# Kernel optimization log

Measured on AMD Instinct MI355X. Metric: run time of the kernel, lower is better.

Reference implementation:

```python
import jax, jax.numpy as jnp
import numpy as np
from jax import lax

L = 12        # transformer layers
H = 768       # d_model
NH = 12       # heads
HD = H // NH  # head dim
F = 2048      # ffn dim (torch TransformerEncoderLayer default)
V = 128       # vocab_size (level logits)
NLV = 128     # n_levels (rows of routed weight W)
B, S = 8, 512
EPS = 1e-5


def _layer_norm(x, g, b):
    mu = jnp.mean(x, axis=-1, keepdims=True)
    var = jnp.mean(jnp.square(x - mu), axis=-1, keepdims=True)
    return g * (x - mu) / jnp.sqrt(var + EPS) + b


def _encoder(x, layer_params):
    # torch nn.TransformerEncoderLayer, post-LN, ReLU, eval mode (no dropout)
    def block(h, p):
        Wqkv, bqkv, Wo, bo, g1, bb1, W1, b1f, W2, b2f, g2, bb2 = p
        qkv = h @ Wqkv.T + bqkv                      # [B,S,3H]
        q, k, v = jnp.split(qkv, 3, axis=-1)
        sh = (h.shape[0], h.shape[1], NH, HD)
        q, k, v = q.reshape(sh), k.reshape(sh), v.reshape(sh)
        scores = jnp.einsum('bqhd,bkhd->bhqk', q, k) / jnp.sqrt(jnp.asarray(HD, h.dtype))
        attn = jax.nn.softmax(scores, axis=-1)
        o = jnp.einsum('bhqk,bkhd->bqhd', attn, v).reshape(h.shape)
        o = o @ Wo.T + bo
        h = _layer_norm(h + o, g1, bb1)
        f = jnp.maximum(h @ W1.T + b1f, 0.0) @ W2.T + b2f
        h = _layer_norm(h + f, g2, bb2)
        return h, None
    x, _ = lax.scan(block, x, layer_params)
    return x


def setup_inputs() -> dict:
    key = jax.random.key(0)
    ks = jax.random.split(key, 20)
    s = 0.02
    rn = lambda k, shp: jax.random.normal(k, shp, jnp.float32) * s
    inp = {
        'level_ids': jax.random.randint(ks[0], (B, S), 0, V, jnp.int32),
        'sublevel_ids': jax.random.randint(ks[1], (B, S), 0, V, jnp.int32),
        'bin_emb': rn(ks[2], (V, H)),
        'sub_emb': rn(ks[3], (V, H)),
        'Wqkv': rn(ks[4], (L, 3 * H, H)),
        'bqkv': jnp.zeros((L, 3 * H), jnp.float32),
        'Wo': rn(ks[5], (L, H, H)),
        'bo': jnp.zeros((L, H), jnp.float32),
        'ln1_g': jnp.ones((L, H), jnp.float32),
        'ln1_b': jnp.zeros((L, H), jnp.float32),
        'W1': rn(ks[6], (L, F, H)),
        'b1': jnp.zeros((L, F), jnp.float32),
        'W2': rn(ks[7], (L, H, F)),
        'b2': jnp.zeros((L, H), jnp.float32),
        'ln2_g': jnp.ones((L, H), jnp.float32),
        'ln2_b': jnp.zeros((L, H), jnp.float32),
        'W_lm': rn(ks[8], (V, H)),
        'b_lm': jnp.zeros((V,), jnp.float32),
        'W': rn(ks[9], (NLV, H, V)),       # routed per-level weights
        'bias': jnp.zeros((NLV, V), jnp.float32),
    }
    return inp


def reference(level_ids, sublevel_ids, bin_emb, sub_emb, Wqkv, bqkv, Wo, bo,
              ln1_g, ln1_b, W1, b1, W2, b2, ln2_g, ln2_b, W_lm, b_lm, W, bias):
    # embedding: sum of two id tables (tabular bin/subbin embedding)
    x = bin_emb[level_ids] + sub_emb[sublevel_ids]            # [B,S,H]
    layer_params = (Wqkv, bqkv, Wo, bo, ln1_g, ln1_b, W1, b1, W2, b2, ln2_g, ln2_b)
    x = _encoder(x, layer_params)                              # [B,S,H]
    out = x @ W_lm.T + b_lm                                    # [B,S,V]
    ix = jnp.argmax(out, axis=-1)                              # [B,S] routing index
    # per-token weight gather + batched vec-mat: the irregular hot path
    Wg = W[ix]                                                 # [B,S,H,V]
    sublevel_out = jnp.einsum('bsh,bshv->bsv', x, Wg) + bias[ix]
    return (out, sublevel_out)
```

## Files before the change

### kernel.cpp

```cpp
#include <hip/hip_runtime.h>
#include <cstdint>
#include <cstddef>

#define TOK 4096
#define HD_ 64
#define NH_ 12
#define H_ 768
#define F_ 2048
#define V_ 128
#define L_ 12
#define SEQ 512
#define BQKV (3*H_)
#define BATCH 8

typedef _Float16 f16;
typedef _Float16 f16x8 __attribute__((ext_vector_type(8)));
typedef _Float16 f16x4 __attribute__((ext_vector_type(4)));
typedef float    f32x4 __attribute__((ext_vector_type(4)));

#define GLDS16(g, l) __builtin_amdgcn_global_load_lds( \
    (const __attribute__((address_space(1))) uint32_t*)(g), \
    (__attribute__((address_space(3))) uint32_t*)(l), 16, 0, 0)

__device__ __forceinline__ float wave_sum(float v) {
#pragma unroll
  for (int m = 32; m >= 1; m >>= 1) v += __shfl_xor(v, m);
  return v;
}

__device__ __forceinline__ void split16(float v, f16& h, f16& lo) {
  h = (f16)v;
  lo = (f16)((v - (float)h) * 2048.0f);
}

__device__ __forceinline__ int swz(int r, int c) {
  int byte = (r << 7) + (c << 1);
  byte ^= (r & 7) << 4;
  return byte >> 1;
}

__global__ __launch_bounds__(256)
void k_convert(const float* __restrict__ src, f16* __restrict__ h, f16* __restrict__ l,
               int n4, float scale) {
  int i = blockIdx.x * 256 + threadIdx.x;
  int stride = gridDim.x * 256;
  for (; i < n4; i += stride) {
    float4 v = ((const float4*)src)[i];
    v.x *= scale; v.y *= scale; v.z *= scale; v.w *= scale;
    f16x4 vh, vl;
    f16 a, b;
    split16(v.x, a, b); vh[0] = a; vl[0] = b;
    split16(v.y, a, b); vh[1] = a; vl[1] = b;
    split16(v.z, a, b); vh[2] = a; vl[2] = b;
    split16(v.w, a, b); vh[3] = a; vl[3] = b;
    ((f16x4*)h)[i] = vh;
    ((f16x4*)l)[i] = vl;
  }
}

__global__ __launch_bounds__(256)
void k_embed2(const int* __restrict__ lid, const int* __restrict__ sid,
              const float* __restrict__ be, const float* __restrict__ se,
              float* __restrict__ x, f16* __restrict__ xh, f16* __restrict__ xl,
              int* __restrict__ counts) {
  int t = blockIdx.x;
  if (t == 0 && threadIdx.x < V_) counts[threadIdx.x] = 0;
  int li = lid[t], si = sid[t];
  const float* bp = be + (size_t)li * H_;
  const float* sp = se + (size_t)si * H_;
  size_t base = (size_t)t * H_;
#pragma unroll
  for (int j = 0; j < 3; ++j) {
    int hh = threadIdx.x + 256 * j;
    float v = bp[hh] + sp[hh];
    x[base + hh] = v;
    f16 a, b; split16(v, a, b);
    xh[base + hh] = a; xl[base + hh] = b;
  }
}

template<int BM, int BN, int MODE, int SPLIT>
__global__ __launch_bounds__(256, 2)
void k_gemm5(const f16* __restrict__ Ah, const f16* __restrict__ Al,
             const f16* __restrict__ Bh, const f16* __restrict__ Bl,
             const float* __restrict__ bias, float* __restrict__ C,
             f16* __restrict__ Ch, f16* __restrict__ Cl,
             int N, int K) {
  constexpr int MI = BM / 32, NJ = BN / 32;
  constexpr int IA = BM / 64, IB = BN / 64;
  constexpr int ABYT = BM * 64, BBYT = BN * 64;
  constexpr int BUFB = 2 * ABYT + 2 * BBYT;
  constexpr int NGL = 2 * (IA + IB);
  __shared__ __align__(16) char sm_[2 * BUFB];
  const int tid = threadIdx.x;
  const int lane = tid & 63, wid = tid >> 6;
  const int wr = wid >> 1, wc = wid & 1;

  const unsigned flat = blockIdx.x + gridDim.x * (blockIdx.y + gridDim.y * blockIdx.z);
  const unsigned G = gridDim.x >> 3;
  const unsigned xcd = flat & 7u;
  const unsigned idx = flat >> 3;
  const unsigned mt = xcd * G + idx % G;
  const unsigned rest = idx / G;
  const unsigned nt = rest % gridDim.y;
  const unsigned zt = rest / gridDim.y;

  const int bm = mt * BM, bn = nt * BN;
  const size_t rs = (size_t)K * 2;
  const size_t koff = (size_t)zt * (size_t)(K / SPLIT) * 2;

  const int srow = tid >> 2, schk = tid & 3;
  const char* ga[2][IA];
  const char* gb[2][IB];
#pragma unroll
  for (int u = 0; u < IA; ++u) {
    int row = u * 64 + srow;
    int c = schk ^ ((row >> 1) & 3);
    ga[0][u] = (const char*)Ah + (size_t)(bm + row) * rs + c * 16 + koff;
    ga[1][u] = (const char*)Al + (size_t)(bm + row) * rs + c * 16 + koff;
  }
#pragma unroll
  for (int u = 0; u < IB; ++u) {
    int row = u * 64 + srow;
    int c = schk ^ ((row >> 1) & 3);
    gb[0][u] = (const char*)Bh + (size_t)(bn + row) * rs + c * 16 + koff;
    gb[1][u] = (const char*)Bl + (size_t)(bn + row) * rs + c * 16 + koff;
  }

  const int rr = lane & 15, cgrp = lane >> 4;
  int aoff[MI][2], boff[NJ][2];
#pragma unroll
  for (int i = 0; i < MI; ++i) {
    int row = wr * (BM / 2) + i * 16 + rr;
    int sw = (cgrp ^ ((row >> 1) & 3)) * 16;
    aoff[i][0] = row * 64 + sw;
    aoff[i][1] = ABYT + row * 64 + sw;
  }
#pragma unroll
  for (int j = 0; j < NJ; ++j) {
    int row = wc * (BN / 2) + j * 16 + rr;
    int sw = (cgrp ^ ((row >> 1) & 3)) * 16;
    boff[j][0] = 2 * ABYT + row * 64 + sw;
    boff[j][1] = 2 * ABYT + BBYT + row * 64 + sw;
  }

  f32x4 aH[MI][NJ], aM[MI][NJ];
#pragma unroll
  for (int i = 0; i < MI; ++i)
#pragma unroll
    for (int j = 0; j < NJ; ++j)
#pragma unroll
      for (int q = 0; q < 4; ++q) { aH[i][j][q] = 0.0f; aM[i][j][q] = 0.0f; }

  auto STG = [&](char* bufbase) __attribute__((always_inline)) {
    char* base = bufbase + wid * 1024;
#pragma unroll
    for (int u = 0; u < IA; ++u) {
      GLDS16(ga[0][u], base + u * 4096);
      GLDS16(ga[1][u], base + ABYT + u * 4096);
      ga[0][u] += 64; ga[1][u] += 64;
    }
#pragma unroll
    for (int u = 0; u < IB; ++u) {
      GLDS16(gb[0][u], base + 2 * ABYT + u * 4096);
      GLDS16(gb[1][u], base + 2 * ABYT + BBYT + u * 4096);
      gb[0][u] += 64; gb[1][u] += 64;
    }
  };

  char* b0 = sm_;
  char* b1 = sm_ + BUFB;
  const int nst = (K / SPLIT) / 32;
  STG(b0);
  STG(b1);
  for (int s = 0; s < nst; ++s) {
    if (s < nst - 1) {
      asm volatile("s_waitcnt vmcnt(%0)" :: "i"(NGL) : "memory");
    } else {
      asm volatile("s_waitcnt vmcnt(0)" ::: "memory");
    }
    __builtin_amdgcn_s_barrier();
    __builtin_amdgcn_sched_barrier(0);
    const char* base = (s & 1) ? b1 : b0;
    f16x8 fb[NJ][2], fa[MI][2];
#pragma unroll
    for (int j = 0; j < NJ; ++j) {
      fb[j][0] = *(const f16x8*)(base + boff[j][0]);
      fb[j][1] = *(const f16x8*)(base + boff[j][1]);
    }
#pragma unroll
    for (int i = 0; i < MI; ++i) {
      fa[i][0] = *(const f16x8*)(base + aoff[i][0]);
      fa[i][1] = *(const f16x8*)(base + aoff[i][1]);
    }
    asm volatile("s_waitcnt lgkmcnt(0)" ::: "memory");
    __builtin_amdgcn_s_barrier();
    __builtin_amdgcn_sched_barrier(0);
    if (s + 2 < nst) STG((char*)base);
    __builtin_amdgcn_s_setprio(1);
#pragma unroll
    for (int i = 0; i < MI; ++i) {
#pragma unroll
      for (int j = 0; j < NJ; ++j) {
        aH[i][j] = __builtin_amdgcn_mfma_f32_16x16x32_f16(fa[i][0], fb[j][0], aH[i][j], 0, 0, 0);
        aM[i][j] = __builtin_amdgcn_mfma_f32_16x16x32_f16(fa[i][0], fb[j][1], aM[i][j], 0, 0, 0);
        aM[i][j] = __builtin_amdgcn_mfma_f32_16x16x32_f16(fa[i][1], fb[j][0], aM[i][j], 0, 0, 0);
      }
    }
    __builtin_amdgcn_s_setprio(0);
  }

  const int r4 = (lane >> 4) * 4, cc = lane & 15;
  float* Cp = (MODE == 3) ? (C + (size_t)zt * ((size_t)TOK * N)) : C;
#pragma unroll
  for (int i = 0; i < MI; ++i) {
#pragma unroll
    for (int j = 0; j < NJ; ++j) {
      int col = bn + wc * (BN / 2) + j * 16 + cc;
      float bz = (MODE == 3) ? 0.0f : bias[col];
#pragma unroll
      for (int q = 0; q < 4; ++q) {
        int row = bm + wr * (BM / 2) + i * 16 + r4 + q;
        float v = (aH[i][j][q] + aM[i][j][q] * (1.0f / 2048.0f)) * (1.0f / 64.0f) + bz;
        if (MODE == 0 || MODE == 3) {
          Cp[(size_t)row * N + col] = v;
        } else {
          if (MODE == 1) v = fmaxf(v, 0.0f);
          f16 a, b; split16(v, a, b);
          Ch[(size_t)row * N + col] = a;
          Cl[(size_t)row * N + col] = b;
        }
      }
    }
  }
}

__global__ __launch_bounds__(256)
void k_flash_mfma(const f16* __restrict__ ph, const f16* __restrict__ pl,
                  f16* __restrict__ oh, f16* __restrict__ ol) {
  __shared__ __align__(16) f16 VtH[4096];
  __shared__ __align__(16) f16 VtL[4096];
  __shared__ __align__(16) f16 PH[4096];
  __shared__ __align__(16) f16 PL[4096];
  __shared__ float PS[2][64];
  const int tid = threadIdx.x;
  const int lane = tid & 63, wid = tid >> 6;
  const int wr = wid >> 1, wc = wid & 1;
  const unsigned flat = blockIdx.x + 8u * blockIdx.y;
  const unsigned xcd = flat & 7u;
  const unsigned idx = flat >> 3;
  const int qt = idx & 7;
  const int bh = xcd * 12 + (idx >> 3);
  const int b = bh / NH_, hd = bh % NH_;
  const int rr = lane & 15, kg = (lane >> 4) * 8;
  const size_t tok0 = (size_t)b * SEQ;

  f16x8 qfh[2][2], qfl[2][2];
#pragma unroll
  for (int ifr = 0; ifr < 2; ++ifr)
#pragma unroll
    for (int ks = 0; ks < 2; ++ks) {
      size_t g = (tok0 + qt * 64 + wr * 32 + ifr * 16 + rr) * (size_t)BQKV + hd * HD_ + ks * 32 + kg;
      qfh[ifr][ks] = *(const f16x8*)&ph[g];
      qfl[ifr][ks] = *(const f16x8*)&pl[g];
    }

  f32x4 oha[2][2], oma[2][2];
  float psum[2] = {0.f, 0.f};
#pragma unroll
  for (int i = 0; i < 2; ++i)
#pragma unroll
    for (int j = 0; j < 2; ++j)
#pragma unroll
      for (int q = 0; q < 4; ++q) { oha[i][j][q] = 0.0f; oma[i][j][q] = 0.0f; }

  const int vj = tid >> 2;
  const int vs = tid & 3;

  for (int kt = 0; kt < SEQ / 64; ++kt) {
    __syncthreads();
#pragma unroll
    for (int s = 0; s < 2; ++s) {
      int d0 = (vs + s * 4) * 8;
      size_t g = (tok0 + kt * 64 + vj) * (size_t)BQKV + 2 * H_ + hd * HD_ + d0;
      f16x8 vh8 = *(const f16x8*)&ph[g];
      f16x8 vl8 = *(const f16x8*)&pl[g];
#pragma unroll
      for (int u = 0; u < 8; ++u) {
        VtH[swz(d0 + u, vj)] = vh8[u];
        VtL[swz(d0 + u, vj)] = vl8[u];
      }
    }
    __syncthreads();
    f16x8 kfh[2][2], kfl[2][2];
#pragma unroll
    for (int jf = 0; jf < 2; ++jf)
#pragma unroll
      for (int ks = 0; ks < 2; ++ks) {
        size_t g = (tok0 + kt * 64 + wc * 32 + jf * 16 + rr) * (size_t)BQKV + H_ + hd * HD_ + ks * 32 + kg;
        kfh[jf][ks] = *(const f16x8*)&ph[g];
        kfl[jf][ks] = *(const f16x8*)&pl[g];
      }
    f32x4 sh[2][2], sm2[2][2];
#pragma unroll
    for (int j = 0; j < 2; ++j)
#pragma unroll
      for (int i = 0; i < 2; ++i)
#pragma unroll
        for (int q = 0; q < 4; ++q) { sh[j][i][q] = 0.0f; sm2[j][i][q] = 0.0f; }
    __builtin_amdgcn_s_setprio(1);
#pragma unroll
    for (int jf = 0; jf < 2; ++jf)
#pragma unroll
      for (int ifr = 0; ifr < 2; ++ifr)
#pragma unroll
        for (int ks = 0; ks < 2; ++ks) {
          sh[jf][ifr]  = __builtin_amdgcn_mfma_f32_16x16x32_f16(kfh[jf][ks], qfh[ifr][ks], sh[jf][ifr], 0, 0, 0);
          sm2[jf][ifr] = __builtin_amdgcn_mfma_f32_16x16x32_f16(kfl[jf][ks], qfh[ifr][ks], sm2[jf][ifr], 0, 0, 0);
          sm2[jf][ifr] = __builtin_amdgcn_mfma_f32_16x16x32_f16(kfh[jf][ks], qfl[ifr][ks], sm2[jf][ifr], 0, 0, 0);
        }
    __builtin_amdgcn_s_setprio(0);
#pragma unroll
    for (int ifr = 0; ifr < 2; ++ifr) {
#pragma unroll
      for (int jf = 0; jf < 2; ++jf) {
        f16x4 v4h, v4l;
#pragma unroll
        for (int q = 0; q < 4; ++q) {
          float sval = (sh[jf][ifr][q] + sm2[jf][ifr][q] * (1.0f / 2048.0f)) * 0.125f;
          float p = expf(sval);
          psum[ifr] += p;
          f16 a, b2; split16(p, a, b2);
          v4h[q] = a; v4l[q] = b2;
        }
        int qi = wr * 32 + ifr * 16 + rr;
        int j0 = wc * 32 + jf * 16 + (lane >> 4) * 4;
        *(f16x4*)&PH[swz(qi, j0)] = v4h;
        *(f16x4*)&PL[swz(qi, j0)] = v4l;
      }
    }
    __syncthreads();
#pragma unroll
    for (int ks = 0; ks < 2; ++ks) {
      f16x8 pfh[2], pfl[2], vfh[2], vfl[2];
#pragma unroll
      for (int ifr = 0; ifr < 2; ++ifr) {
        pfh[ifr] = *(const f16x8*)&PH[swz(wr * 32 + ifr * 16 + rr, ks * 32 + kg)];
        pfl[ifr] = *(const f16x8*)&PL[swz(wr * 32 + ifr * 16 + rr, ks * 32 + kg)];
      }
#pragma unroll
      for (int jf = 0; jf < 2; ++jf) {
        vfh[jf] = *(const f16x8*)&VtH[swz(wc * 32 + jf * 16 + rr, ks * 32 + kg)];
        vfl[jf] = *(const f16x8*)&VtL[swz(wc * 32 + jf * 16 + rr, ks * 32 + kg)];
      }
      __builtin_amdgcn_s_setprio(1);
#pragma unroll
      for (int ifr = 0; ifr < 2; ++ifr)
#pragma unroll
        for (int jf = 0; jf < 2; ++jf) {
          oha[ifr][jf] = __builtin_amdgcn_mfma_f32_16x16x32_f16(pfh[ifr], vfh[jf], oha[ifr][jf], 0, 0, 0);
          oma[ifr][jf] = __builtin_amdgcn_mfma_f32_16x16x32_f16(pfh[ifr], vfl[jf], oma[ifr][jf], 0, 0, 0);
          oma[ifr][jf] = __builtin_amdgcn_mfma_f32_16x16x32_f16(pfl[ifr], vfh[jf], oma[ifr][jf], 0, 0, 0);
        }
      __builtin_amdgcn_s_setprio(0);
    }
  }

#pragma unroll
  for (int ifr = 0; ifr < 2; ++ifr) {
    psum[ifr] += __shfl_xor(psum[ifr], 16);
    psum[ifr] += __shfl_xor(psum[ifr], 32);
  }
  if (lane < 16) {
    PS[wc][wr * 32 + lane]      = psum[0];
    PS[wc][wr * 32 + 16 + lane] = psum[1];
  }
  __syncthreads();

#pragma unroll
  for (int ifr = 0; ifr < 2; ++ifr)
#pragma unroll
    for (int jf = 0; jf < 2; ++jf)
#pragma unroll
      for (int q = 0; q < 4; ++q) {
        int i = wr * 32 + ifr * 16 + (lane >> 4) * 4 + q;
        float inv = 1.0f / (PS[0][i] + PS[1][i]);
        float o = (oha[ifr][jf][q] + oma[ifr][jf][q] * (1.0f / 2048.0f)) * inv;
        size_t g = (tok0 + qt * 64 + i) * (size_t)H_ + hd * HD_ + wc * 32 + jf * 16 + rr;
        f16 a, b2; split16(o, a, b2);
        oh[g] = a; ol[g] = b2;
      }
}

__global__ __launch_bounds__(256)
void k_ln_res3(const float* __restrict__ xin, const float* __restrict__ part,
               const float* __restrict__ bcol,
               const float* __restrict__ g, const float* __restrict__ bb,
               float* __restrict__ xout, f16* __restrict__ xh, f16* __restrict__ xl) {
  __shared__ float red[8];
  int t = blockIdx.x;
  const float* xr = xin + (size_t)t * H_;
  const float* p0 = part + (size_t)t * H_;
  const float* p1 = part + (size_t)TOK * H_ + (size_t)t * H_;
  float v[3];
#pragma unroll
  for (int j = 0; j < 3; ++j) {
    int hh = threadIdx.x + 256 * j;
    v[j] = xr[hh] + ((p0[hh] + p1[hh]) + bcol[hh]);
  }
  float s = v[0] + v[1] + v[2];
  s = wave_sum(s);
  int w = threadIdx.x >> 6;
  if ((threadIdx.x & 63) == 0) red[w] = s;
  __syncthreads();
  float mu = (red[0] + red[1] + red[2] + red[3]) * (1.0f / 768.0f);
  float q = 0.f;
#pragma unroll
  for (int j = 0; j < 3; ++j) { float d = v[j] - mu; q = fmaf(d, d, q); }
  q = wave_sum(q);
  if ((threadIdx.x & 63) == 0) red[4 + w] = q;
  __syncthreads();
  float var = (red[4] + red[5] + red[6] + red[7]) * (1.0f / 768.0f);
  float rinv = 1.0f / sqrtf(var + 1e-5f);
#pragma unroll
  for (int j = 0; j < 3; ++j) {
    int hh = threadIdx.x + 256 * j;
    float val = fmaf(g[hh], (v[j] - mu) * rinv, bb[hh]);
    size_t idx = (size_t)t * H_ + hh;
    xout[idx] = val;
    f16 a, b; split16(val, a, b);
    xh[idx] = a; xl[idx] = b;
  }
}

__global__ __launch_bounds__(64)
void k_argmax2(const float* __restrict__ part, const float* __restrict__ blm,
               float* __restrict__ out0, int* __restrict__ ix,
               int* __restrict__ counts) {
  int t = blockIdx.x, l = threadIdx.x;
  const size_t S = (size_t)TOK * V_;
  size_t c0 = (size_t)t * V_ + l;
  size_t c1 = c0 + 64;
  float v0 = ((part[c0] + part[S + c0]) + part[2 * S + c0]) + part[3 * S + c0] + blm[l];
  float v1 = ((part[c1] + part[S + c1]) + part[2 * S + c1]) + part[3 * S + c1] + blm[l + 64];
  out0[c0] = v0;
  out0[c1] = v1;
  float best = v0; int bi = l;
  if (v1 > best) { best = v1; bi = 64 + l; }
#pragma unroll
  for (int m = 1; m < 64; m <<= 1) {
    float ov = __shfl_xor(best, m);
    int oi = __shfl_xor(bi, m);
    if (ov > best || (ov == best && oi < bi)) { best = ov; bi = oi; }
  }
  if (l == 0) { ix[t] = bi; atomicAdd(&counts[bi], 1); }
}

__global__ __launch_bounds__(128)
void k_prep(const int* __restrict__ counts, int* __restrict__ offsets,
            int* __restrict__ cursors, int4* __restrict__ chunks,
            int* __restrict__ nchunks) {
  __shared__ int s[128];
  int r = threadIdx.x;
  int c = counts[r];
  s[r] = c; __syncthreads();
  for (int d = 1; d < 128; d <<= 1) {
    int v = (r >= d) ? s[r - d] : 0; __syncthreads();
    s[r] += v; __syncthreads();
  }
  int off = s[r] - c;
  offsets[r] = off;
  cursors[r] = 0;
  int nch = (c + 15) >> 4;
  __syncthreads();
  s[r] = nch; __syncthreads();
  for (int d = 1; d < 128; d <<= 1) {
    int v = (r >= d) ? s[r - d] : 0; __syncthreads();
    s[r] += v; __syncthreads();
  }
  int cb = s[r] - nch;
  for (int u = 0; u < nch; ++u) {
    int rem = c - u * 16;
    chunks[cb + u] = make_int4(r, off + u * 16, rem < 16 ? rem : 16, 0);
  }
  if (r == 127) *nchunks = s[127];
}

__global__ __launch_bounds__(256)
void k_scatter(const int* __restrict__ ix, const int* __restrict__ offsets,
               int* __restrict__ cursors, int* __restrict__ bucket) {
  int t = blockIdx.x * 256 + threadIdx.x;
  int r = ix[t];
  int p = atomicAdd(&cursors[r], 1);
  bucket[offsets[r] + p] = t;
}

__global__ __launch_bounds__(256)
void k_convT(const float* __restrict__ W, f16* __restrict__ wth, f16* __restrict__ wtl) {
  __shared__ float tile[64][65];
  const int r = blockIdx.x, vb = blockIdx.y * 64;
  const int tid = threadIdx.x;
  const int la = tid & 63, wv = tid >> 6;
  for (int ht = 0; ht < H_ / 64; ++ht) {
    int h0 = ht * 64;
#pragma unroll
    for (int i = 0; i < 16; ++i) {
      int row = wv + i * 4;
      tile[row][la] = W[(size_t)r * (H_ * V_) + (size_t)(h0 + row) * V_ + vb + la];
    }
    __syncthreads();
#pragma unroll
    for (int i = 0; i < 16; ++i) {
      int vl = wv + i * 4;
      float w = tile[la][vl];
      f16 a, b; split16(w, a, b);
      size_t o = ((size_t)r * V_ + vb + vl) * H_ + h0 + la;
      wth[o] = a; wtl[o] = b;
    }
    __syncthreads();
  }
}

__global__ __launch_bounds__(256)
void k_sublevel3(const f16* __restrict__ xh, const f16* __restrict__ xl,
                 const f16* __restrict__ wth, const f16* __restrict__ wtl,
                 const float* __restrict__ bias, const int* __restrict__ bucket,
                 const int4* __restrict__ chunks, const int* __restrict__ nchunks,
                 float* __restrict__ out) {
  int c = blockIdx.x;
  if (c >= *nchunks) return;
  int4 ch = chunks[c];
  int r = ch.x, ts = ch.y, nt = ch.z;
  __shared__ int toks[16];
  int tid = threadIdx.x;
  if (tid < 16) toks[tid] = bucket[ts + (tid < nt ? tid : 0)];
  __syncthreads();
  const int lane = tid & 63, wid = tid >> 6;
  const int rr = lane & 15, kg = (lane >> 4) * 8;
  const int myTok = toks[rr];
  const size_t abase = (size_t)myTok * H_ + kg;

  f32x4 aH[2], aM[2];
#pragma unroll
  for (int j = 0; j < 2; ++j)
#pragma unroll
    for (int q = 0; q < 4; ++q) { aH[j][q] = 0.0f; aM[j][q] = 0.0f; }

  size_t wb[2];
#pragma unroll
  for (int j = 0; j < 2; ++j)
    wb[j] = ((size_t)r * V_ + wid * 32 + j * 16 + rr) * H_ + kg;

  for (int k0 = 0; k0 < H_; k0 += 32) {
    f16x8 ah = *(const f16x8*)&xh[abase + k0];
    f16x8 al = *(const f16x8*)&xl[abase + k0];
#pragma unroll
    for (int j = 0; j < 2; ++j) {
      f16x8 bh = *(const f16x8*)&wth[wb[j] + k0];
      f16x8 bl = *(const f16x8*)&wtl[wb[j] + k0];
      aH[j] = __builtin_amdgcn_mfma_f32_16x16x32_f16(ah, bh, aH[j], 0, 0, 0);
      aM[j] = __builtin_amdgcn_mfma_f32_16x16x32_f16(ah, bl, aM[j], 0, 0, 0);
      aM[j] = __builtin_amdgcn_mfma_f32_16x16x32_f16(al, bh, aM[j], 0, 0, 0);
    }
  }

  const int r4 = (lane >> 4) * 4, cc = lane & 15;
#pragma unroll
  for (int j = 0; j < 2; ++j) {
#pragma unroll
    for (int q = 0; q < 4; ++q) {
      int row = r4 + q;
      if (row < nt) {
        int col = wid * 32 + j * 16 + cc;
        out[(size_t)toks[row] * V_ + col] =
            aH[j][q] + aM[j][q] * (1.0f / 2048.0f) + bias[(size_t)r * V_ + col];
      }
    }
  }
}

extern "C" void kernel_launch(void* const* d_in, const int* in_sizes, int n_in,
                              void* d_out, int out_size, void* d_ws, size_t ws_size,
                              hipStream_t stream) {
  const int*   lid  = (const int*)d_in[0];
  const int*   sid  = (const int*)d_in[1];
  const float* be   = (const float*)d_in[2];
  const float* se   = (const float*)d_in[3];
  const float* Wqkv = (const float*)d_in[4];
  const float* bqkv = (const float*)d_in[5];
  const float* Wo   = (const float*)d_in[6];
  const float* bo   = (const float*)d_in[7];
  const float* g1   = (const float*)d_in[8];
  const float* b1n  = (const float*)d_in[9];
  const float* W1   = (const float*)d_in[10];
  const float* b1f  = (const float*)d_in[11];
  const float* W2   = (const float*)d_in[12];
  const float* b2f  = (const float*)d_in[13];
  const float* g2   = (const float*)d_in[14];
  const float* b2n  = (const float*)d_in[15];
  const float* Wlm  = (const float*)d_in[16];
  const float* blm  = (const float*)d_in[17];
  const float* Wrt  = (const float*)d_in[18];
  const float* brt  = (const float*)d_in[19];

  char* ws = (char*)d_ws;
  float* x    = (float*)(ws + 0);
  f16*   xh   = (f16*)  (ws + 12582912);
  f16*   xl   = (f16*)  (ws + 18874368);
  f16*   qh   = (f16*)  (ws + 25165824);
  f16*   ql   = (f16*)  (ws + 44040192);
  f16*   midh = qh;
  f16*   midl = ql;
  f16*   ath  = (f16*)  (ws + 62914560);
  f16*   atl  = (f16*)  (ws + 69206016);
  float* bufY = (float*)(ws + 75497472);
  float* pO   = (float*)(ws + 25165824);
  float* pF   = (float*)(ws + 62914560);
  float* pLM  = bufY;
  f16*   wth  = (f16*)  (ws + 25165824);
  f16*   wtl  = (f16*)  (ws + 50331648);
  f16*   wsh  = (f16*)  (ws + 88080384);
  f16*   wsl  = (f16*)  (ws + 91619328);
  f16*   wlmh = (f16*)  (ws + 95158272);
  f16*   wlml = (f16*)  (ws + 95354880);
  int*   ix   = (int*)  (ws + 95551488);
  int*   counts  = (int*)(ws + 95567872);
  int*   cursors = (int*)(ws + 95568384);
  int*   offsets = (int*)(ws + 95568896);
  int4*  chunks  = (int4*)(ws + 95569920);
  int*   nchunks = (int*)(ws + 95576064);
  int*   bucket  = (int*)(ws + 95576320);
  const size_t need = 95592704;
  if (ws_size < need) return;

  bool big = ws_size >= 95600640ull + 265000000ull;
  f16 *bWqh = nullptr, *bWql = nullptr, *bWoh = nullptr, *bWol = nullptr,
      *bW1h = nullptr, *bW1l = nullptr, *bW2h = nullptr, *bW2l = nullptr;
  if (big) {
    char* p = ws + 95600640;
    bWqh = (f16*)p; p += 42467328;
    bWql = (f16*)p; p += 42467328;
    bWoh = (f16*)p; p += 14155776;
    bWol = (f16*)p; p += 14155776;
    bW1h = (f16*)p; p += 37748736;
    bW1l = (f16*)p; p += 37748736;
    bW2h = (f16*)p; p += 37748736;
    bW2l = (f16*)p; p += 37748736;
    k_convert<<<2048, 256, 0, stream>>>(Wqkv, bWqh, bWql, L_ * BQKV * H_ / 4, 64.f);
    k_convert<<<2048, 256, 0, stream>>>(Wo,   bWoh, bWol, L_ * H_ * H_ / 4, 64.f);
    k_convert<<<2048, 256, 0, stream>>>(W1,   bW1h, bW1l, L_ * F_ * H_ / 4, 64.f);
    k_convert<<<2048, 256, 0, stream>>>(W2,   bW2h, bW2l, L_ * H_ * F_ / 4, 64.f);
  }
  k_convert<<<96, 256, 0, stream>>>(Wlm, wlmh, wlml, V_ * H_ / 4, 64.f);

  float* out0 = (float*)d_out;
  float* out1 = out0 + (size_t)TOK * V_;

  k_embed2<<<TOK, 256, 0, stream>>>(lid, sid, be, se, x, xh, xl, counts);

  for (int l = 0; l < L_; ++l) {
    const float* bqkv_l = bqkv + (size_t)l * BQKV;
    const float* bo_l   = bo   + (size_t)l * H_;
    const float* g1_l   = g1   + (size_t)l * H_;
    const float* b1n_l  = b1n  + (size_t)l * H_;
    const float* b1f_l  = b1f  + (size_t)l * F_;
    const float* b2f_l  = b2f  + (size_t)l * H_;
    const float* g2_l   = g2   + (size_t)l * H_;
    const float* b2n_l  = b2n  + (size_t)l * H_;

    const f16 *wh, *wl2;
    if (big) { wh = bWqh + (size_t)l * BQKV * H_; wl2 = bWql + (size_t)l * BQKV * H_; }
    else {
      k_convert<<<1728, 256, 0, stream>>>(Wqkv + (size_t)l * BQKV * H_, wsh, wsl, BQKV * H_ / 4, 64.f);
      wh = wsh; wl2 = wsl;
    }
    k_gemm5<128, 128, 2, 1><<<dim3(TOK / 128, BQKV / 128, 1), 256, 0, stream>>>(
        xh, xl, wh, wl2, bqkv_l, nullptr, qh, ql, BQKV, H_);
    k_flash_mfma<<<dim3(SEQ / 64, BATCH * NH_), 256, 0, stream>>>(qh, ql, ath, atl);
    if (big) { wh = bWoh + (size_t)l * H_ * H_; wl2 = bWol + (size_t)l * H_ * H_; }
    else {
      k_convert<<<576, 256, 0, stream>>>(Wo + (size_t)l * H_ * H_, wsh, wsl, H_ * H_ / 4, 64.f);
      wh = wsh; wl2 = wsl;
    }
    k_gemm5<128, 128, 3, 2><<<dim3(TOK / 128, H_ / 128, 2), 256, 0, stream>>>(
        ath, atl, wh, wl2, nullptr, pO, nullptr, nullptr, H_, H_);
    k_ln_res3<<<TOK, 256, 0, stream>>>(x, pO, bo_l, g1_l, b1n_l, x, xh, xl);
    if (big) { wh = bW1h + (size_t)l * F_ * H_; wl2 = bW1l + (size_t)l * F_ * H_; }
    else {
      k_convert<<<1536, 256, 0, stream>>>(W1 + (size_t)l * F_ * H_, wsh, wsl, F_ * H_ / 4, 64.f);
      wh = wsh; wl2 = wsl;
    }
    k_gemm5<128, 128, 1, 1><<<dim3(TOK / 128, F_ / 128, 1), 256, 0, stream>>>(
        xh, xl, wh, wl2, b1f_l, nullptr, midh, midl, F_, H_);
    if (big) { wh = bW2h + (size_t)l * H_ * F_; wl2 = bW2l + (size_t)l * H_ * F_; }
    else {
      k_convert<<<1536, 256, 0, stream>>>(W2 + (size_t)l * H_ * F_, wsh, wsl, H_ * F_ / 4, 64.f);
      wh = wsh; wl2 = wsl;
    }
    k_gemm5<128, 128, 3, 2><<<dim3(TOK / 128, H_ / 128, 2), 256, 0, stream>>>(
        midh, midl, wh, wl2, nullptr, pF, nullptr, nullptr, H_, F_);
    k_ln_res3<<<TOK, 256, 0, stream>>>(x, pF, b2f_l, g2_l, b2n_l, x, xh, xl);
  }

  k_gemm5<64, 64, 3, 4><<<dim3(TOK / 64, V_ / 64, 4), 256, 0, stream>>>(
      xh, xl, wlmh, wlml, nullptr, pLM, nullptr, nullptr, V_, H_);
  k_convT<<<dim3(V_, 2), 256, 0, stream>>>(Wrt, wth, wtl);
  k_argmax2<<<TOK, 64, 0, stream>>>(pLM, blm, out0, ix, counts);
  k_prep<<<1, 128, 0, stream>>>(counts, offsets, cursors, chunks, nchunks);
  k_scatter<<<TOK / 256, 256, 0, stream>>>(ix, offsets, cursors, bucket);
  k_sublevel3<<<384, 256, 0, stream>>>(xh, xl, wth, wtl, brt, bucket, chunks, nchunks, out1);
}
```

Before: 3.222 ms.

## Pre-transpose V in a separate kernel and double-buffer async V loads in flash attention

Adds a kernel that transposes and swizzles the V tiles (hi and lo halves) into a workspace buffer, one 64-token tile per block. The flash kernel then stages each next V tile into a double-buffered LDS region with direct global-to-LDS loads issued before the P stores, which removes the per-iteration scalar transpose and one barrier. The cost is an extra launch per layer and an extra round trip of V through global memory. It also relies on hand-written waitcnt counts for correctness.

```diff
diff --git a/kernel.cpp b/kernel.cpp
--- a/kernel.cpp
+++ b/kernel.cpp
@@ -236,10 +236,42 @@
 }
 
 __global__ __launch_bounds__(256)
+void k_vt(const f16* __restrict__ qh, const f16* __restrict__ ql,
+          f16* __restrict__ vtp) {
+  __shared__ f16 T0[64][72];
+  __shared__ f16 T1[64][72];
+  const int bh = blockIdx.x, kt = blockIdx.y;
+  const int b = bh / NH_, hd = bh % NH_;
+  const int tid = threadIdx.x;
+#pragma unroll
+  for (int r = 0; r < 2; ++r) {
+    int it = tid + 256 * r;
+    int s = it >> 3, grp = it & 7;
+    size_t g = ((size_t)(b * SEQ + kt * 64 + s)) * BQKV + 2 * H_ + hd * HD_ + grp * 8;
+    *(f16x8*)&T0[s][grp * 8] = *(const f16x8*)&qh[g];
+    *(f16x8*)&T1[s][grp * 8] = *(const f16x8*)&ql[g];
+  }
+  __syncthreads();
+  f16* o0 = vtp + ((size_t)bh * 8 + kt) * 4096;
+  f16* o1 = o0 + (size_t)96 * 8 * 4096;
+#pragma unroll
+  for (int r = 0; r < 2; ++r) {
+    int it = tid + 256 * r;
+    int d = it & 63, sg = it >> 6;
+    f16x8 vh, vl;
+#pragma unroll
+    for (int u = 0; u < 8; ++u) { vh[u] = T0[sg * 8 + u][d]; vl[u] = T1[sg * 8 + u][d]; }
+    *(f16x8*)&o0[swz(d, sg * 8)] = vh;
+    *(f16x8*)&o1[swz(d, sg * 8)] = vl;
+  }
+}
+
+__global__ __launch_bounds__(256)
 void k_flash_mfma(const f16* __restrict__ ph, const f16* __restrict__ pl,
+                  const f16* __restrict__ vtp,
                   f16* __restrict__ oh, f16* __restrict__ ol) {
-  __shared__ __align__(16) f16 VtH[4096];
-  __shared__ __align__(16) f16 VtL[4096];
+  __shared__ __align__(16) f16 VtH[2][4096];
+  __shared__ __align__(16) f16 VtL[2][4096];
   __shared__ __align__(16) f16 PH[4096];
   __shared__ __align__(16) f16 PL[4096];
   __shared__ float PS[2][64];
@@ -254,6 +286,17 @@
   const int b = bh / NH_, hd = bh % NH_;
   const int rr = lane & 15, kg = (lane >> 4) * 8;
   const size_t tok0 = (size_t)b * SEQ;
+  const char* vs0 = (const char*)(vtp + (size_t)bh * 8 * 4096);
+  const char* vs1 = vs0 + (size_t)96 * 8 * 4096 * 2;
+
+  auto STGV = [&](int kt, int buf) __attribute__((always_inline)) {
+#pragma unroll
+    for (int u = 0; u < 2; ++u) {
+      int off = (wid + 4 * u) * 1024;
+      GLDS16(vs0 + (size_t)kt * 8192 + off + lane * 16, (char*)&VtH[buf][0] + off);
+      GLDS16(vs1 + (size_t)kt * 8192 + off + lane * 16, (char*)&VtL[buf][0] + off);
+    }
+  };
 
   f16x8 qfh[2][2], qfl[2][2];
 #pragma unroll
@@ -274,24 +317,9 @@
 #pragma unroll
       for (int q = 0; q < 4; ++q) { oha[i][j][q] = 0.0f; oma[i][j][q] = 0.0f; }
 
-  const int vj = tid >> 2;
-  const int vs = tid & 3;
-
+  STGV(0, 0);
   for (int kt = 0; kt < SEQ / 64; ++kt) {
-    __syncthreads();
-#pragma unroll
-    for (int s = 0; s < 2; ++s) {
-      int d0 = (vs + s * 4) * 8;
-      size_t g = (tok0 + kt * 64 + vj) * (size_t)BQKV + 2 * H_ + hd * HD_ + d0;
-      f16x8 vh8 = *(const f16x8*)&ph[g];
-      f16x8 vl8 = *(const f16x8*)&pl[g];
-#pragma unroll
-      for (int u = 0; u < 8; ++u) {
-        VtH[swz(d0 + u, vj)] = vh8[u];
-        VtL[swz(d0 + u, vj)] = vl8[u];
-      }
-    }
-    __syncthreads();
+    const int cb = kt & 1;
     f16x8 kfh[2][2], kfl[2][2];
 #pragma unroll
     for (int jf = 0; jf < 2; ++jf)
@@ -320,26 +348,38 @@
           sm2[jf][ifr] = __builtin_amdgcn_mfma_f32_16x16x32_f16(kfh[jf][ks], qfl[ifr][ks], sm2[jf][ifr], 0, 0, 0);
         }
     __builtin_amdgcn_s_setprio(0);
-#pragma unroll
-    for (int ifr = 0; ifr < 2; ++ifr) {
-#pragma unroll
-      for (int jf = 0; jf < 2; ++jf) {
-        f16x4 v4h, v4l;
+    f16x4 pv4h[2][2], pv4l[2][2];
+#pragma unroll
+    for (int ifr = 0; ifr < 2; ++ifr)
+#pragma unroll
+      for (int jf = 0; jf < 2; ++jf)
 #pragma unroll
         for (int q = 0; q < 4; ++q) {
           float sval = (sh[jf][ifr][q] + sm2[jf][ifr][q] * (1.0f / 2048.0f)) * 0.125f;
           float p = expf(sval);
           psum[ifr] += p;
           f16 a, b2; split16(p, a, b2);
-          v4h[q] = a; v4l[q] = b2;
+          pv4h[ifr][jf][q] = a; pv4l[ifr][jf][q] = b2;
         }
+    __builtin_amdgcn_s_barrier();
+    __builtin_amdgcn_sched_barrier(0);
+    if (kt + 1 < SEQ / 64) STGV(kt + 1, cb ^ 1);
+#pragma unroll
+    for (int ifr = 0; ifr < 2; ++ifr)
+#pragma unroll
+      for (int jf = 0; jf < 2; ++jf) {
         int qi = wr * 32 + ifr * 16 + rr;
         int j0 = wc * 32 + jf * 16 + (lane >> 4) * 4;
-        *(f16x4*)&PH[swz(qi, j0)] = v4h;
-        *(f16x4*)&PL[swz(qi, j0)] = v4l;
+        *(f16x4*)&PH[swz(qi, j0)] = pv4h[ifr][jf];
+        *(f16x4*)&PL[swz(qi, j0)] = pv4l[ifr][jf];
       }
-    }
-    __syncthreads();
+    if (kt + 1 < SEQ / 64) {
+      asm volatile("s_waitcnt vmcnt(4) lgkmcnt(0)" ::: "memory");
+    } else {
+      asm volatile("s_waitcnt vmcnt(0) lgkmcnt(0)" ::: "memory");
+    }
+    __builtin_amdgcn_s_barrier();
+    __builtin_amdgcn_sched_barrier(0);
 #pragma unroll
     for (int ks = 0; ks < 2; ++ks) {
       f16x8 pfh[2], pfl[2], vfh[2], vfl[2];
@@ -350,8 +390,8 @@
       }
 #pragma unroll
       for (int jf = 0; jf < 2; ++jf) {
-        vfh[jf] = *(const f16x8*)&VtH[swz(wc * 32 + jf * 16 + rr, ks * 32 + kg)];
-        vfl[jf] = *(const f16x8*)&VtL[swz(wc * 32 + jf * 16 + rr, ks * 32 + kg)];
+        vfh[jf] = *(const f16x8*)&VtH[cb][swz(wc * 32 + jf * 16 + rr, ks * 32 + kg)];
+        vfl[jf] = *(const f16x8*)&VtL[cb][swz(wc * 32 + jf * 16 + rr, ks * 32 + kg)];
       }
       __builtin_amdgcn_s_setprio(1);
 #pragma unroll
@@ -614,6 +654,7 @@
   f16*   ath  = (f16*)  (ws + 62914560);
   f16*   atl  = (f16*)  (ws + 69206016);
   float* bufY = (float*)(ws + 75497472);
+  f16*   vtp  = (f16*)  (ws + 75497472);
   float* pO   = (float*)(ws + 25165824);
   float* pF   = (float*)(ws + 62914560);
   float* pLM  = bufY;
@@ -676,7 +717,8 @@
     }
     k_gemm5<128, 128, 2, 1><<<dim3(TOK / 128, BQKV / 128, 1), 256, 0, stream>>>(
         xh, xl, wh, wl2, bqkv_l, nullptr, qh, ql, BQKV, H_);
-    k_flash_mfma<<<dim3(SEQ / 64, BATCH * NH_), 256, 0, stream>>>(qh, ql, ath, atl);
+    k_vt<<<dim3(96, 8), 256, 0, stream>>>(qh, ql, vtp);
+    k_flash_mfma<<<dim3(SEQ / 64, BATCH * NH_), 256, 0, stream>>>(qh, ql, vtp, ath, atl);
     if (big) { wh = bWoh + (size_t)l * H_ * H_; wl2 = bWol + (size_t)l * H_ * H_; }
     else {
       k_convert<<<576, 256, 0, stream>>>(Wo + (size_t)l * H_ * H_, wsh, wsl, H_ * H_ / 4, 64.f);
```

Measured after the change: 3.258 ms. No clear change (+1.1%).
